# Kernel optimization log

Hardware: AMD Instinct MI355X
Metric: run time of the kernel (lower is better)

The kernel has to match this reference:

```python
import jax, jax.numpy as jnp
import numpy as np
import math

B, T, E, H = 4, 2048, 1024, 16
ALPHA = 32.0


def setup_inputs() -> dict:
    key = jax.random.key(0)
    ks = jax.random.split(key, 6)
    s = 1.0 / math.sqrt(E)
    return {
        "x": jax.random.normal(ks[0], (B, T, E), dtype=jnp.float32),
        "ch_list": 0,
        "Wq": jax.random.normal(ks[1], (E, E), dtype=jnp.float32) * s,
        "bq": jnp.zeros((E,), jnp.float32),
        "Wk": jax.random.normal(ks[2], (E, E), dtype=jnp.float32) * s,
        "bk": jnp.zeros((E,), jnp.float32),
        "Wv": jax.random.normal(ks[3], (E, E), dtype=jnp.float32) * s,
        "bv": jnp.zeros((E,), jnp.float32),
        "Wp": jax.random.normal(ks[4], (E, E), dtype=jnp.float32) * s,
        "bp": jnp.zeros((E,), jnp.float32),
    }


def reference(x, ch_list, Wq, bq, Wk, bk, Wv, bv, Wp, bp):
    Bx, Tx, Ex = x.shape
    hd = Ex // H  # head dim
    # linear projections (weights stored [in, out]); split heads -> [B,H,T,hd]
    def heads(W, b):
        return (x @ W + b).reshape(Bx, Tx, H, hd).transpose(0, 2, 1, 3)
    q, k, v = heads(Wq, bq), heads(Wk, bk), heads(Wv, bv)
    scale = 1.0 / (ALPHA * math.sqrt(hd))
    qk = jnp.einsum("bhqd,bhkd->bhqk", q * scale, k)  # [B,H,T,T]
    # extra max-rescale BEFORE the causal mask (faithful to original order)
    qk = qk - jnp.max(qk, axis=-1, keepdims=True)
    causal = jnp.tril(jnp.ones((Tx, Tx), dtype=bool))  # [T,T]
    qk = jnp.where(causal[None, None], qk, -jnp.inf)
    att = jax.nn.softmax(qk * ALPHA, axis=-1)  # dropout p=0 -> identity
    y = jnp.einsum("bhqk,bhkd->bhqd", att, v)
    y = y.transpose(0, 2, 1, 3).reshape(Bx, Tx, Ex)
    return y @ Wp + bp
```

## Files before the change

### kernel.cpp

```cpp
#include <hip/hip_runtime.h>
#include <cmath>

typedef unsigned short u16;
typedef unsigned int u32;
typedef __bf16 bf16x8 __attribute__((ext_vector_type(8)));
typedef float  floatx4 __attribute__((ext_vector_type(4)));
typedef float  floatx16 __attribute__((ext_vector_type(16)));
typedef unsigned int u32x4 __attribute__((ext_vector_type(4)));

#define T_DIM 2048
#define E_DIM 1024
#define H_DIM 16
#define HD    64
#define M_DIM 8192
#define NE    8388608
#define E2    1048576
#define QSCALE 0.18033688f

__device__ __forceinline__ u16 f2bf(float f) {
    unsigned u = __builtin_bit_cast(unsigned, f);
    return (u16)((u + 0x7FFFu + ((u >> 16) & 1u)) >> 16);
}
__device__ __forceinline__ u32 pack2bf(float f0, float f1) {
    u32 a0 = __builtin_bit_cast(u32, f0) + 0x8000u;
    u32 a1 = __builtin_bit_cast(u32, f1) + 0x8000u;
    return __builtin_amdgcn_perm(a1, a0, 0x07060302u);
}

__device__ __forceinline__ void gl_lds16(const u16* g, const u16* l) {
    __builtin_amdgcn_global_load_lds(
        (const __attribute__((address_space(1))) void*)g,
        (__attribute__((address_space(3))) void*)l,
        16, 0, 0);
}

__device__ __forceinline__ bf16x8 ld_frag(const u16* p) {
    return *(const bf16x8*)p;
}

#define S_BARRIER()  asm volatile("s_barrier" ::: "memory")
#define WAIT_LGKM0() asm volatile("s_waitcnt lgkmcnt(0)" ::: "memory")

__global__ void cvt_x_kernel(const float* __restrict__ x, u16* __restrict__ xb) {
    const size_t i = (size_t)blockIdx.x * 256 + threadIdx.x;
    const float4* s = (const float4*)x + i * 2;
    const float4 a = s[0], b = s[1];
    u16 v[8] __attribute__((aligned(16)));
    v[0]=f2bf(a.x); v[1]=f2bf(a.y); v[2]=f2bf(a.z); v[3]=f2bf(a.w);
    v[4]=f2bf(b.x); v[5]=f2bf(b.y); v[6]=f2bf(b.z); v[7]=f2bf(b.w);
    *(uint4*)(xb + i * 8) = *(const uint4*)v;
}

__global__ void transpose_cvt_kernel(const float* __restrict__ w0, const float* __restrict__ w1,
                                     const float* __restrict__ w2, const float* __restrict__ w3,
                                     u16* __restrict__ out) {
    __shared__ u16 tile[64][65];
    const float* W = blockIdx.z == 0 ? w0 : blockIdx.z == 1 ? w1 : blockIdx.z == 2 ? w2 : w3;
    u16* O = out + (size_t)blockIdx.z * E2;
    const int k0 = blockIdx.y * 64, n0 = blockIdx.x * 64;
    const int r = threadIdx.x >> 2, cp = (threadIdx.x & 3) * 16;
    const float4* src = (const float4*)&W[(size_t)(k0 + r) * E_DIM + n0 + cp];
    #pragma unroll
    for (int j4 = 0; j4 < 4; ++j4) {
        const float4 f = src[j4];
        tile[r][cp + j4*4 + 0] = f2bf(f.x);
        tile[r][cp + j4*4 + 1] = f2bf(f.y);
        tile[r][cp + j4*4 + 2] = f2bf(f.z);
        tile[r][cp + j4*4 + 3] = f2bf(f.w);
    }
    __syncthreads();
    u16 vals[16] __attribute__((aligned(16)));
    #pragma unroll
    for (int j = 0; j < 16; ++j) vals[j] = tile[cp + j][r];
    u16* dst = &O[(size_t)(n0 + r) * E_DIM + k0 + cp];
    *(uint4*)dst       = *(const uint4*)vals;
    *(uint4*)(dst + 8) = *(const uint4*)(vals + 8);
}

#define NT 16

#define MFMA_Q(F0)                                                              \
    _Pragma("unroll") for (int kk = 0; kk < 2; ++kk)                            \
    _Pragma("unroll") for (int mi = 0; mi < 4; ++mi)                            \
    _Pragma("unroll") for (int ni = 0; ni < 2; ++ni)                            \
        acc[(F0)+mi][ni] = __builtin_amdgcn_mfma_f32_16x16x32_bf16(             \
            Aq[mi][kk], Bq[ni][kk], acc[(F0)+mi][ni], 0, 0, 0);

template<int REMAP>
__global__ __launch_bounds__(512, 2)
void gemm256_kernel(const u16* __restrict__ A, const u16* __restrict__ Bt,
                    const float* __restrict__ bias0, const float* __restrict__ bias1,
                    const float* __restrict__ bias2, void* __restrict__ outp,
                    u16* __restrict__ vtp)
{
    __shared__ u16 SM[49152];
    const int tid = threadIdx.x;
    const int w = tid >> 6, lane = tid & 63, quad = lane >> 4, l15 = lane & 15;
    const int wm = w >> 2, wn = w & 3;

    const int nbx = (REMAP == 1) ? 24 : 8;
    const int cpx = gridDim.x >> 3;
    const int swz = ((int)blockIdx.x & 7) * cpx + ((int)blockIdx.x >> 3);
    const int bx = swz % nbx, by = swz / nbx;
    const int r0 = by * 256, c0 = bx * 128;

    const u16* pA[2]; const u16* pB[2]; unsigned lb[2];
    #pragma unroll
    for (int i = 0; i < 2; ++i) {
        const int L = i * 512 + tid, ur = L >> 3, sl = L & 7, c = sl ^ (ur & 7);
        const int ra = ((ur >> 6) << 7) + (ur & 63);
        pA[i] = A  + (size_t)(r0 + ra) * E_DIM + c * 8;
        pB[i] = Bt + (size_t)(c0 + ur) * E_DIM + c * 8;
        lb[i] = (unsigned)i * 8192u + (unsigned)w * 1024u;
    }
    auto stageA = [&](int kt, int u) {
        #pragma unroll
        for (int i = 0; i < 2; ++i) {
            const unsigned off = __builtin_amdgcn_readfirstlane(
                (unsigned)(kt & 1) * 32768u + (unsigned)u * 16384u + lb[i]);
            gl_lds16(pA[i] + u * (64 * E_DIM) + kt * 64,
                     (const u16*)((const char*)SM + off));
        }
    };
    auto stageB = [&](int kt) {
        #pragma unroll
        for (int i = 0; i < 2; ++i) {
            const unsigned off = __builtin_amdgcn_readfirstlane(
                65536u + (unsigned)(kt & 1) * 16384u + lb[i]);
            gl_lds16(pB[i] + kt * 64,
                     (const u16*)((const char*)SM + off));
        }
    };

    const int arow = (wm * 64 + l15) * 64;
    const int brow = (wn * 32 + l15) * 64;
    const int sl0  = (quad ^ (l15 & 7)) * 8;

    floatx4 acc[8][2];
    #pragma unroll
    for (int f = 0; f < 8; ++f)
        #pragma unroll
        for (int n = 0; n < 2; ++n) acc[f][n] = (floatx4){0.f, 0.f, 0.f, 0.f};

    bf16x8 Aq[4][2], Bq[2][2];

    stageA(0, 0); stageA(0, 1); stageB(0);
    stageA(1, 0); stageB(1);
    asm volatile("s_waitcnt vmcnt(4)" ::: "memory");
    S_BARRIER();

    for (int kt = 0; kt < NT; ++kt) {
        const unsigned Ab = (unsigned)(kt & 1) * 16384u;
        const unsigned Bb = 32768u + (unsigned)(kt & 1) * 8192u;

        #pragma unroll
        for (int mi = 0; mi < 4; ++mi) {
            Aq[mi][0] = ld_frag(&SM[Ab + arow + mi * 1024 + sl0]);
            Aq[mi][1] = ld_frag(&SM[Ab + arow + mi * 1024 + (sl0 ^ 32)]);
        }
        #pragma unroll
        for (int ni = 0; ni < 2; ++ni) {
            Bq[ni][0] = ld_frag(&SM[Bb + brow + ni * 1024 + sl0]);
            Bq[ni][1] = ld_frag(&SM[Bb + brow + ni * 1024 + (sl0 ^ 32)]);
        }
        if (kt + 1 < NT) stageA(kt + 1, 1);
        S_BARRIER(); WAIT_LGKM0();
        __builtin_amdgcn_s_setprio(1);
        MFMA_Q(0)
        __builtin_amdgcn_s_setprio(0);
        asm volatile("s_waitcnt vmcnt(6)" ::: "memory");
        S_BARRIER();

        #pragma unroll
        for (int mi = 0; mi < 4; ++mi) {
            Aq[mi][0] = ld_frag(&SM[Ab + 8192 + arow + mi * 1024 + sl0]);
            Aq[mi][1] = ld_frag(&SM[Ab + 8192 + arow + mi * 1024 + (sl0 ^ 32)]);
        }
        if (kt + 2 < NT) { stageA(kt + 2, 0); stageB(kt + 2); }
        S_BARRIER(); WAIT_LGKM0();
        __builtin_amdgcn_s_setprio(1);
        MFMA_Q(4)
        __builtin_amdgcn_s_setprio(0);
        if (kt < NT - 2)       asm volatile("s_waitcnt vmcnt(6)" ::: "memory");
        else if (kt == NT - 2) asm volatile("s_waitcnt vmcnt(0)" ::: "memory");
        S_BARRIER();
    }

    #pragma unroll
    for (int n = 0; n < 2; ++n) {
        const int col = c0 + wn * 32 + n * 16 + l15;
        if (REMAP == 1) {
            const int which = col >> 10, cc = col & 1023;
            const float* bp_ = which == 0 ? bias0 : which == 1 ? bias1 : bias2;
            const float bv = bp_[cc];
            const int h = cc >> 6, d = cc & 63;
            #pragma unroll
            for (int f = 0; f < 8; ++f) {
                const int row0 = r0 + wm * 128 + f * 16 + quad * 4;
                const int b = row0 >> 11, t0 = row0 & (T_DIM - 1);
                if (which == 2) {
                    uint2 pk;
                    pk.x = pack2bf(acc[f][n][0] + bv, acc[f][n][1] + bv);
                    pk.y = pack2bf(acc[f][n][2] + bv, acc[f][n][3] + bv);
                    *(uint2*)&vtp[((size_t)((b * H_DIM + h) * HD + d)) * T_DIM + t0] = pk;
                } else {
                    #pragma unroll
                    for (int r = 0; r < 4; ++r) {
                        float val = acc[f][n][r] + bv;
                        if (which == 0) val *= QSCALE;
                        ((u16*)outp)[(size_t)which * NE +
                            (((size_t)(b * H_DIM + h) * T_DIM + (t0 + r)) * HD + d)] = f2bf(val);
                    }
                }
            }
        } else {
            const float bv = bias0[col];
            #pragma unroll
            for (int f = 0; f < 8; ++f) {
                #pragma unroll
                for (int r = 0; r < 4; ++r) {
                    const int row = r0 + wm * 128 + f * 16 + quad * 4 + r;
                    ((float*)outp)[(size_t)row * E_DIM + col] = acc[f][n][r] + bv;
                }
            }
        }
    }
}

__global__ __launch_bounds__(256, 2)
void attn_kernel(const u16* __restrict__ q, const u16* __restrict__ k,
                 const u16* __restrict__ vt, u16* __restrict__ y)
{
    __shared__ u16 Ks[2][128 * 64];
    __shared__ u16 Vs[2][64 * 128];

    const int tid = threadIdx.x;
    const int w = tid >> 6, lane = tid & 63;
    const int hl = lane >> 5, l31 = lane & 31, l7 = lane & 7;
    const int bh = blockIdx.x;
    const int qt = gridDim.y - 1 - blockIdx.y;
    const int q0 = qt * 128;
    const int b = bh >> 4, h = bh & (H_DIM - 1);
    const size_t qkb = (size_t)bh * (T_DIM * HD);
    const size_t vtb = (size_t)bh * (HD * T_DIM);

    const int qrow = q0 + w * 32 + l31;
    bf16x8 Qf[4];
    #pragma unroll
    for (int kc = 0; kc < 4; ++kc)
        Qf[kc] = ld_frag(&q[qkb + (size_t)qrow * HD + kc * 16 + hl * 8]);

    float rsum = 0.f;
    floatx16 O[2];
    #pragma unroll
    for (int i = 0; i < 16; ++i) { O[0][i] = 0.f; O[1][i] = 0.f; }

    auto stage = [&](int jt, int sel) {
        const int j0 = jt * 128;
        #pragma unroll
        for (int i = 0; i < 4; ++i) {
            const int L = i * 256 + tid;
            const unsigned off = __builtin_amdgcn_readfirstlane(i * 4096 + w * 1024);
            {   const int row = L >> 3, ch = (L & 7) ^ (row & 7);
                gl_lds16(&k[qkb + (size_t)(j0 + row) * HD + ch * 8],
                         (u16*)((char*)&Ks[sel][0] + off)); }
            {   const int row = L >> 4, ch = (L & 15) ^ (row & 7);
                gl_lds16(&vt[vtb + (size_t)row * T_DIM + j0 + ch * 8],
                         (u16*)((char*)&Vs[sel][0] + off)); }
        }
    };

    stage(0, 0);
    for (int jt = 0; jt <= qt; ++jt) {
        __syncthreads();
        if (jt < qt) stage(jt + 1, (jt + 1) & 1);
        const u16* const Kb = &Ks[jt & 1][0];
        const u16* const Vb = &Vs[jt & 1][0];

        const bool diag = (jt == qt);
        const int nkg = diag ? (w + 1) : 4;

        #pragma unroll
        for (int kg = 0; kg < 4; ++kg) {
            if (kg < nkg) {
                floatx16 S;
                #pragma unroll
                for (int i = 0; i < 16; ++i) S[i] = 0.f;
                const int krow = kg * 32 + l31;
                #pragma unroll
                for (int kc = 0; kc < 4; ++kc) {
                    const int ch = (kc * 2 + hl) ^ l7;
                    S = __builtin_amdgcn_mfma_f32_32x32x16_bf16(
                            ld_frag(&Kb[krow * 64 + ch * 8]), Qf[kc], S, 0, 0, 0);
                }

                const bool bnd = diag && (kg == w);
                u32 u[8], ru[8];
                #pragma unroll
                for (int i = 0; i < 8; ++i) {
                    const int row0 = (2*i & 3) + 8 * (i >> 1) + 4 * hl;
                    float p0 = __builtin_amdgcn_exp2f(S[2*i]);
                    float p1 = __builtin_amdgcn_exp2f(S[2*i + 1]);
                    if (bnd && (row0     > l31)) p0 = 0.f;
                    if (bnd && (row0 + 1 > l31)) p1 = 0.f;
                    rsum += p0 + p1;
                    u[i] = pack2bf(p0, p1);
                }
                #pragma unroll
                for (int i = 0; i < 8; ++i) ru[i] = __shfl_xor(u[i], 32, 64);
                const u32x4 f0 = hl ? (u32x4){ru[2], ru[3], u[2], u[3]}
                                    : (u32x4){u[0], u[1], ru[0], ru[1]};
                const u32x4 f1 = hl ? (u32x4){ru[6], ru[7], u[6], u[7]}
                                    : (u32x4){u[4], u[5], ru[4], ru[5]};

                #pragma unroll
                for (int c2 = 0; c2 < 2; ++c2) {
                    const bf16x8 Pf = __builtin_bit_cast(bf16x8, c2 ? f1 : f0);
                    const int kc16 = kg * 4 + c2 * 2 + hl;
                    #pragma unroll
                    for (int dh = 0; dh < 2; ++dh) {
                        const int d = dh * 32 + l31;
                        const int ch = kc16 ^ l7;
                        O[dh] = __builtin_amdgcn_mfma_f32_32x32x16_bf16(
                                    Pf, ld_frag(&Vb[d * 128 + ch * 8]), O[dh], 0, 0, 0);
                    }
                }
            }
        }
    }

    rsum += __shfl_xor(rsum, 32, 64);
    const float linv = 1.0f / rsum;
    #pragma unroll
    for (int i = 0; i < 16; ++i) {
        const int qr = (i & 3) + 8 * (i >> 2) + 4 * hl;
        const float lq = __shfl(linv, qr, 32);
        const int t = q0 + w * 32 + qr;
        const size_t base = ((size_t)(b * T_DIM + t)) * E_DIM + h * HD;
        y[base + l31]      = f2bf(O[0][i] * lq);
        y[base + 32 + l31] = f2bf(O[1][i] * lq);
    }
}

extern "C" void kernel_launch(void* const* d_in, const int* in_sizes, int n_in,
                              void* d_out, int out_size, void* d_ws, size_t ws_size,
                              hipStream_t stream)
{
    const float* x  = (const float*)d_in[0];
    const float* Wq = (const float*)d_in[2];
    const float* bq = (const float*)d_in[3];
    const float* Wk = (const float*)d_in[4];
    const float* bk = (const float*)d_in[5];
    const float* Wv = (const float*)d_in[6];
    const float* bv = (const float*)d_in[7];
    const float* Wp = (const float*)d_in[8];
    const float* bp = (const float*)d_in[9];

    u16* xb  = (u16*)d_ws;
    u16* wt  = xb + NE;
    u16* qb  = wt + 4 * (size_t)E2;
    u16* kb  = qb + NE;
    u16* vtb = kb + NE;
    u16* yb  = vtb + NE;

    cvt_x_kernel<<<NE / (256 * 8), 256, 0, stream>>>(x, xb);
    transpose_cvt_kernel<<<dim3(16, 16, 4), 256, 0, stream>>>(Wq, Wk, Wv, Wp, wt);
    gemm256_kernel<1><<<768, 512, 0, stream>>>(xb, wt, bq, bk, bv, qb, vtb);
    attn_kernel<<<dim3(64, 16), 256, 0, stream>>>(qb, kb, vtb, yb);
    gemm256_kernel<0><<<256, 512, 0, stream>>>(yb, wt + 3 * (size_t)E2, bp, bp, bp, (float*)d_out, nullptr);
}
```

Baseline: 248.0 us.

## Restructure GEMM to 4-wave blocks with 128x64 warp tiles and triple-buffered K=32 stages

Rewrites the bf16 GEMM kernel to use 256 threads (4 waves) per 256x128 block instead of 512, so each wave computes a 128x64 tile with more MFMA reuse per fragment load. The K step drops from 64 to 32 and the LDS pipeline becomes a three-slot ring, prefetching two steps ahead. This aims to raise the MFMA-to-LDS-read ratio and deepen latency hiding. In exchange it raises accumulator register pressure and leaves fewer waves per CU to hide latency.

```diff
diff --git a/kernel.cpp b/kernel.cpp
--- a/kernel.cpp
+++ b/kernel.cpp
@@ -77,26 +77,25 @@
     *(uint4*)(dst + 8) = *(const uint4*)(vals + 8);
 }
 
-#define NT 16
-
-#define MFMA_Q(F0)                                                              \
-    _Pragma("unroll") for (int kk = 0; kk < 2; ++kk)                            \
-    _Pragma("unroll") for (int mi = 0; mi < 4; ++mi)                            \
-    _Pragma("unroll") for (int ni = 0; ni < 2; ++ni)                            \
-        acc[(F0)+mi][ni] = __builtin_amdgcn_mfma_f32_16x16x32_bf16(             \
-            Aq[mi][kk], Bq[ni][kk], acc[(F0)+mi][ni], 0, 0, 0);
+#define NT 32
+
+#define MFMA_PH(H)                                                              \
+    _Pragma("unroll") for (int j = 0; j < 4; ++j)                               \
+    _Pragma("unroll") for (int n = 0; n < 4; ++n)                               \
+        acc[(H)*4 + j][n] = __builtin_amdgcn_mfma_f32_16x16x32_bf16(            \
+            Aq[j], Bq[n], acc[(H)*4 + j][n], 0, 0, 0);
 
 template<int REMAP>
-__global__ __launch_bounds__(512, 2)
+__global__ __launch_bounds__(256, 2)
 void gemm256_kernel(const u16* __restrict__ A, const u16* __restrict__ Bt,
                     const float* __restrict__ bias0, const float* __restrict__ bias1,
                     const float* __restrict__ bias2, void* __restrict__ outp,
                     u16* __restrict__ vtp)
 {
-    __shared__ u16 SM[49152];
+    __shared__ u16 SM[36864];
     const int tid = threadIdx.x;
     const int w = tid >> 6, lane = tid & 63, quad = lane >> 4, l15 = lane & 15;
-    const int wm = w >> 2, wn = w & 3;
+    const int wm = w >> 1, wn = w & 1;
 
     const int nbx = (REMAP == 1) ? 24 : 8;
     const int cpx = gridDim.x >> 3;
@@ -104,91 +103,85 @@
     const int bx = swz % nbx, by = swz / nbx;
     const int r0 = by * 256, c0 = bx * 128;
 
-    const u16* pA[2]; const u16* pB[2]; unsigned lb[2];
+    const u16* pA[4]; const u16* pB[2];
+    #pragma unroll
+    for (int i = 0; i < 4; ++i) {
+        const int L = i * 256 + tid, ra = L >> 2, ca = (L & 3) ^ (ra & 3);
+        pA[i] = A + (size_t)(r0 + ra) * E_DIM + ca * 8;
+    }
     #pragma unroll
     for (int i = 0; i < 2; ++i) {
-        const int L = i * 512 + tid, ur = L >> 3, sl = L & 7, c = sl ^ (ur & 7);
-        const int ra = ((ur >> 6) << 7) + (ur & 63);
-        pA[i] = A  + (size_t)(r0 + ra) * E_DIM + c * 8;
-        pB[i] = Bt + (size_t)(c0 + ur) * E_DIM + c * 8;
-        lb[i] = (unsigned)i * 8192u + (unsigned)w * 1024u;
-    }
-    auto stageA = [&](int kt, int u) {
+        const int L = i * 256 + tid, rb = L >> 2, cb = (L & 3) ^ (rb & 3);
+        pB[i] = Bt + (size_t)(c0 + rb) * E_DIM + cb * 8;
+    }
+    auto stageA = [&](int kt, int slot) {
+        #pragma unroll
+        for (int i = 0; i < 4; ++i) {
+            const unsigned off = __builtin_amdgcn_readfirstlane(
+                (unsigned)slot * 16384u + (unsigned)i * 4096u + (unsigned)w * 1024u);
+            gl_lds16(pA[i] + kt * 32, (const u16*)((const char*)SM + off));
+        }
+    };
+    auto stageB = [&](int kt, int slot) {
         #pragma unroll
         for (int i = 0; i < 2; ++i) {
             const unsigned off = __builtin_amdgcn_readfirstlane(
-                (unsigned)(kt & 1) * 32768u + (unsigned)u * 16384u + lb[i]);
-            gl_lds16(pA[i] + u * (64 * E_DIM) + kt * 64,
-                     (const u16*)((const char*)SM + off));
+                49152u + (unsigned)slot * 8192u + (unsigned)i * 4096u + (unsigned)w * 1024u);
+            gl_lds16(pB[i] + kt * 32, (const u16*)((const char*)SM + off));
         }
     };
-    auto stageB = [&](int kt) {
-        #pragma unroll
-        for (int i = 0; i < 2; ++i) {
-            const unsigned off = __builtin_amdgcn_readfirstlane(
-                65536u + (unsigned)(kt & 1) * 16384u + lb[i]);
-            gl_lds16(pB[i] + kt * 64,
-                     (const u16*)((const char*)SM + off));
-        }
-    };
-
-    const int arow = (wm * 64 + l15) * 64;
-    const int brow = (wn * 32 + l15) * 64;
-    const int sl0  = (quad ^ (l15 & 7)) * 8;
-
-    floatx4 acc[8][2];
+
+    const int sl0 = (quad ^ (l15 & 3)) * 8;
+    const int arow = (wm * 128 + l15) * 32;
+    const int brow = (wn * 64 + l15) * 32;
+
+    floatx4 acc[8][4];
     #pragma unroll
     for (int f = 0; f < 8; ++f)
         #pragma unroll
-        for (int n = 0; n < 2; ++n) acc[f][n] = (floatx4){0.f, 0.f, 0.f, 0.f};
-
-    bf16x8 Aq[4][2], Bq[2][2];
-
-    stageA(0, 0); stageA(0, 1); stageB(0);
-    stageA(1, 0); stageB(1);
-    asm volatile("s_waitcnt vmcnt(4)" ::: "memory");
+        for (int n = 0; n < 4; ++n) acc[f][n] = (floatx4){0.f, 0.f, 0.f, 0.f};
+
+    bf16x8 Aq[4], Bq[4];
+
+    stageA(0, 0); stageB(0, 0);
+    stageA(1, 1); stageB(1, 1);
+    asm volatile("s_waitcnt vmcnt(6)" ::: "memory");
     S_BARRIER();
 
+    int scur = 0, sstg = 2;
     for (int kt = 0; kt < NT; ++kt) {
-        const unsigned Ab = (unsigned)(kt & 1) * 16384u;
-        const unsigned Bb = 32768u + (unsigned)(kt & 1) * 8192u;
-
-        #pragma unroll
-        for (int mi = 0; mi < 4; ++mi) {
-            Aq[mi][0] = ld_frag(&SM[Ab + arow + mi * 1024 + sl0]);
-            Aq[mi][1] = ld_frag(&SM[Ab + arow + mi * 1024 + (sl0 ^ 32)]);
-        }
-        #pragma unroll
-        for (int ni = 0; ni < 2; ++ni) {
-            Bq[ni][0] = ld_frag(&SM[Bb + brow + ni * 1024 + sl0]);
-            Bq[ni][1] = ld_frag(&SM[Bb + brow + ni * 1024 + (sl0 ^ 32)]);
-        }
-        if (kt + 1 < NT) stageA(kt + 1, 1);
+        const unsigned Au = (unsigned)scur * 8192u;
+        const unsigned Bu = 24576u + (unsigned)scur * 4096u;
+
+        #pragma unroll
+        for (int j = 0; j < 4; ++j) Aq[j] = ld_frag(&SM[Au + arow + j * 512 + sl0]);
+        #pragma unroll
+        for (int n = 0; n < 4; ++n) Bq[n] = ld_frag(&SM[Bu + brow + n * 512 + sl0]);
+        if (kt + 2 < NT) stageA(kt + 2, sstg);
         S_BARRIER(); WAIT_LGKM0();
         __builtin_amdgcn_s_setprio(1);
-        MFMA_Q(0)
+        MFMA_PH(0)
         __builtin_amdgcn_s_setprio(0);
-        asm volatile("s_waitcnt vmcnt(6)" ::: "memory");
         S_BARRIER();
 
         #pragma unroll
-        for (int mi = 0; mi < 4; ++mi) {
-            Aq[mi][0] = ld_frag(&SM[Ab + 8192 + arow + mi * 1024 + sl0]);
-            Aq[mi][1] = ld_frag(&SM[Ab + 8192 + arow + mi * 1024 + (sl0 ^ 32)]);
-        }
-        if (kt + 2 < NT) { stageA(kt + 2, 0); stageB(kt + 2); }
+        for (int j = 0; j < 4; ++j) Aq[j] = ld_frag(&SM[Au + arow + 2048 + j * 512 + sl0]);
+        if (kt + 2 < NT) stageB(kt + 2, sstg);
         S_BARRIER(); WAIT_LGKM0();
         __builtin_amdgcn_s_setprio(1);
-        MFMA_Q(4)
+        MFMA_PH(1)
         __builtin_amdgcn_s_setprio(0);
         if (kt < NT - 2)       asm volatile("s_waitcnt vmcnt(6)" ::: "memory");
         else if (kt == NT - 2) asm volatile("s_waitcnt vmcnt(0)" ::: "memory");
         S_BARRIER();
-    }
-
-    #pragma unroll
-    for (int n = 0; n < 2; ++n) {
-        const int col = c0 + wn * 32 + n * 16 + l15;
+
+        scur = scur == 2 ? 0 : scur + 1;
+        sstg = sstg == 2 ? 0 : sstg + 1;
+    }
+
+    #pragma unroll
+    for (int n = 0; n < 4; ++n) {
+        const int col = c0 + wn * 64 + n * 16 + l15;
         if (REMAP == 1) {
             const int which = col >> 10, cc = col & 1023;
             const float* bp_ = which == 0 ? bias0 : which == 1 ? bias1 : bias2;
@@ -365,7 +358,7 @@
 
     cvt_x_kernel<<<NE / (256 * 8), 256, 0, stream>>>(x, xb);
     transpose_cvt_kernel<<<dim3(16, 16, 4), 256, 0, stream>>>(Wq, Wk, Wv, Wp, wt);
-    gemm256_kernel<1><<<768, 512, 0, stream>>>(xb, wt, bq, bk, bv, qb, vtb);
+    gemm256_kernel<1><<<768, 256, 0, stream>>>(xb, wt, bq, bk, bv, qb, vtb);
     attn_kernel<<<dim3(64, 16), 256, 0, stream>>>(qb, kb, vtb, yb);
-    gemm256_kernel<0><<<256, 512, 0, stream>>>(yb, wt + 3 * (size_t)E2, bp, bp, bp, (float*)d_out, nullptr);
-}
+    gemm256_kernel<0><<<256, 256, 0, stream>>>(yb, wt + 3 * (size_t)E2, bp, bp, bp, (float*)d_out, nullptr);
+}
```

After: 247.8 us. About the same (-0.1%).
